# Kernel optimization log

Hardware: AMD Instinct MI355X
Metric: run time of the kernel (lower is better)

## Reference

```python
import jax, jax.numpy as jnp
import numpy as np

NUM_LAYER = 5
EMB = 256
N = 100000
E = 300000
SELF_LOOP_BOND = 4
BN_EPS = 1e-5


def setup_inputs() -> dict:
    key = jax.random.key(0)
    ks = jax.random.split(key, 16)
    f = lambda k, shape: jax.random.normal(k, shape, jnp.float32) * 0.02
    return {
        "x_atom": jax.random.randint(ks[0], (N,), 0, 120),
        "x_chir": jax.random.randint(ks[1], (N,), 0, 3),
        "edge_index": jax.random.randint(ks[2], (2, E), 0, N),
        "edge_bond": jax.random.randint(ks[3], (E,), 0, 4),
        "edge_dir": jax.random.randint(ks[4], (E,), 0, 3),
        "atom_emb": f(ks[5], (120, EMB)),
        "chir_emb": f(ks[6], (3, EMB)),
        "bond_embs": f(ks[7], (NUM_LAYER, 6, EMB)),
        "dir_embs": f(ks[8], (NUM_LAYER, 3, EMB)),
        "W1s": f(ks[9], (NUM_LAYER, 2 * EMB, EMB)),
        "b1s": f(ks[10], (NUM_LAYER, 2 * EMB)),
        "W2s": f(ks[11], (NUM_LAYER, EMB, 2 * EMB)),
        "b2s": f(ks[12], (NUM_LAYER, EMB)),
        "bn_w": jnp.ones((NUM_LAYER, EMB), jnp.float32),
        "bn_b": jnp.zeros((NUM_LAYER, EMB), jnp.float32),
    }


def reference(x_atom, x_chir, edge_index, edge_bond, edge_dir,
              atom_emb, chir_emb, bond_embs, dir_embs,
              W1s, b1s, W2s, b2s, bn_w, bn_b):
    n = x_atom.shape[0]
    src, dst = edge_index[0], edge_index[1]
    # add self loops (edge_attr = [4, 0] for each node)
    loop = jnp.arange(n)
    src_full = jnp.concatenate([src, loop])          # [E+N]
    dst_full = jnp.concatenate([dst, loop])          # [E+N]
    bond_full = jnp.concatenate([edge_bond, jnp.full((n,), SELF_LOOP_BOND, edge_bond.dtype)])
    dir_full = jnp.concatenate([edge_dir, jnp.zeros((n,), edge_dir.dtype)])

    # initial node features: atom + chirality embeddings
    h = atom_emb[x_atom] + chir_emb[x_chir]          # [N, EMB]

    for l in range(NUM_LAYER):
        # per-layer edge embeddings (bond type + bond direction)
        e_emb = bond_embs[l][bond_full] + dir_embs[l][dir_full]   # [E+N, EMB]
        # message = x_j + edge_attr; aggregate = scatter-add to dst
        msg = h[src_full] + e_emb                                  # gather
        agg = jax.ops.segment_sum(msg, dst_full, num_segments=n)  # scatter-add
        # update MLP: Linear(EMB->2EMB) -> ReLU -> Linear(2EMB->EMB)
        hmid = jax.nn.relu(agg @ W1s[l].T + b1s[l])                # [N, 2EMB]
        h2 = hmid @ W2s[l].T + b2s[l]                              # [N, EMB]
        # batch norm (training mode: batch statistics, biased variance)
        mean = h2.mean(axis=0)
        var = h2.var(axis=0)
        h2 = (h2 - mean) * jax.lax.rsqrt(var + BN_EPS) * bn_w[l] + bn_b[l]
        # relu on all but last layer; dropout with p=0 is identity
        if l < NUM_LAYER - 1:
            h2 = jax.nn.relu(h2)
        h = h2
    # JK == 'last'
    return h
```

## Files before the change

kernel.cpp:

```cpp
#include <hip/hip_runtime.h>

#define EMB 256
#define NLAYER 5
#define CHUNK 1024

typedef unsigned int u32;
typedef unsigned short u16;

typedef __bf16 bf16x8 __attribute__((ext_vector_type(8)));
typedef float f32x4 __attribute__((ext_vector_type(4)));

__device__ __forceinline__ float bf2f(u16 u) {
    union { u32 i; float f; } x; x.i = ((u32)u) << 16; return x.f;
}
__device__ __forceinline__ u16 f2bf(float f) {
    union { float f; u32 i; } x; x.f = f;
    u32 r = x.i + 0x7FFFu + ((x.i >> 16) & 1u);
    return (u16)(r >> 16);
}
__device__ __forceinline__ u32 cvt_pk_bf16(float lo, float hi) {
    u32 r;
    asm("v_cvt_pk_bf16_f32 %0, %1, %2" : "=v"(r) : "v"(lo), "v"(hi));
    return r;
}
__device__ __forceinline__ void unpack4(uint2 p, float* o) {
    union { u32 i; float f; } a, b, c, d;
    a.i = p.x << 16; b.i = p.x & 0xFFFF0000u;
    c.i = p.y << 16; d.i = p.y & 0xFFFF0000u;
    o[0] = a.f; o[1] = b.f; o[2] = c.f; o[3] = d.f;
}

#define GLOAD(dst, ptr) asm volatile("global_load_dwordx4 %0, %1, off" : "=&v"(dst) : "v"(ptr))
#define VMWAIT(n) asm volatile("s_waitcnt vmcnt(" #n ")" ::: "memory")

__global__ void k_detect(const u32* __restrict__ bnw_raw, int* __restrict__ flag) {
    if (threadIdx.x == 0 && blockIdx.x == 0)
        *flag = (bnw_raw[0] == 0x3F803F80u) ? 1 : 0;
}

struct Cvt { const void* s; u16* d; int n; };
struct CvtTab { Cvt t[10]; };

__global__ void k_convert(CvtTab tab, const int* __restrict__ flag, int maxn) {
    int f = *flag;
    int stride = gridDim.x * blockDim.x;
    for (int i = blockIdx.x * blockDim.x + threadIdx.x; i < maxn; i += stride) {
        for (int j = 0; j < 10; j++) {
            if (i < tab.t[j].n) {
                u16 v;
                if (f) v = ((const u16*)tab.t[j].s)[i];
                else   v = f2bf(((const float*)tab.t[j].s)[i]);
                tab.t[j].d[i] = v;
            }
        }
    }
}

__global__ void k_zero(u32* p, int n) {
    int i = blockIdx.x * blockDim.x + threadIdx.x;
    if (i < n) p[i] = 0u;
}

__global__ void k_hist(const int* __restrict__ eidx, const int* __restrict__ ebond,
                       const int* __restrict__ edir,
                       u32* __restrict__ cnt, u32* __restrict__ cntb, u32* __restrict__ cntd, int E) {
    int e = blockIdx.x * blockDim.x + threadIdx.x;
    if (e >= E) return;
    int dst = eidx[E + e];
    atomicAdd(&cnt[dst], 1u);
    atomicAdd(&cntb[dst * 4 + ebond[e]], 1u);
    atomicAdd(&cntd[dst * 3 + edir[e]], 1u);
}

__global__ void k_chunksum(const u32* __restrict__ cnt, u32* __restrict__ partial, int N) {
    int b = blockIdx.x, t = threadIdx.x;
    int base = b * CHUNK + t * 4;
    u32 s = 0;
    for (int i = 0; i < 4; i++) { int idx = base + i; if (idx < N) s += cnt[idx]; }
    __shared__ u32 red[256];
    red[t] = s; __syncthreads();
    for (int o = 128; o > 0; o >>= 1) { if (t < o) red[t] += red[t + o]; __syncthreads(); }
    if (t == 0) partial[b] = red[0];
}

__global__ void k_scanpartial(u32* partial, u32* indptr, int nch, int N) {
    if (threadIdx.x == 0 && blockIdx.x == 0) {
        u32 run = 0;
        for (int i = 0; i < nch; i++) { u32 x = partial[i]; partial[i] = run; run += x; }
        indptr[N] = run;
    }
}

__global__ void k_chunkscan(const u32* __restrict__ cnt, const u32* __restrict__ partial,
                            u32* __restrict__ indptr, u32* __restrict__ fillp, int N) {
    int b = blockIdx.x, t = threadIdx.x;
    int base = b * CHUNK + t * 4;
    u32 c[4]; u32 tsum = 0;
    for (int i = 0; i < 4; i++) { int idx = base + i; c[i] = (idx < N) ? cnt[idx] : 0u; tsum += c[i]; }
    __shared__ u32 sc[256];
    sc[t] = tsum; __syncthreads();
    for (int o = 1; o < 256; o <<= 1) {
        u32 x = (t >= o) ? sc[t - o] : 0u;
        __syncthreads();
        sc[t] += x;
        __syncthreads();
    }
    u32 run = partial[b] + sc[t] - tsum;
    for (int i = 0; i < 4; i++) {
        int idx = base + i;
        if (idx < N) { indptr[idx] = run; fillp[idx] = run; }
        run += c[i];
    }
}

__global__ void k_fill(const int* __restrict__ eidx, u32* __restrict__ fillp,
                       u32* __restrict__ srcs, int E) {
    int e = blockIdx.x * blockDim.x + threadIdx.x;
    if (e >= E) return;
    int dst = eidx[E + e];
    u32 pos = atomicAdd(&fillp[dst], 1u);
    srcs[pos] = (u32)eidx[e];
}

__global__ void k_h0(const int* __restrict__ xa, const int* __restrict__ xc,
                     const u16* __restrict__ aemb, const u16* __restrict__ cemb,
                     u16* __restrict__ H, int N) {
    int wave = threadIdx.x >> 6, lane = threadIdx.x & 63;
    int v = blockIdx.x * 4 + wave;
    if (v >= N) return;
    int a = xa[v], c = xc[v];
    int c4 = lane * 4;
    uint2 pa = *(const uint2*)(aemb + (size_t)a * EMB + c4);
    uint2 pc = *(const uint2*)(cemb + (size_t)c * EMB + c4);
    float fa[4], fc[4];
    unpack4(pa, fa); unpack4(pc, fc);
    ushort4 ov;
    ov.x = f2bf(fa[0] + fc[0]); ov.y = f2bf(fa[1] + fc[1]);
    ov.z = f2bf(fa[2] + fc[2]); ov.w = f2bf(fa[3] + fc[3]);
    *(ushort4*)(H + (size_t)v * EMB + c4) = ov;
}

#define KP 264
#define HSS 272

#define ACCROW(P)                                                     \
    {                                                                 \
        float f_[4]; unpack4(P, f_);                                  \
        _Pragma("unroll") for (int k_ = 0; k_ < 4; k_++) {            \
            float y_ = f_[k_] * sc[k_] + sh[k_];                      \
            if (relu) y_ = fmaxf(y_, 0.f);                            \
            acc[k_] += y_;                                            \
        }                                                             \
    }

#define G1STEP(BUF)                                                                              \
    {                                                                                            \
        _Pragma("unroll") for (int j = 0; j < 4; j++)                                            \
            _Pragma("unroll") for (int i = 0; i < 4; i++)                                        \
                acc1[i][j] = __builtin_amdgcn_mfma_f32_16x16x32_bf16(BUF[j], af[i], acc1[i][j], 0, 0, 0); \
        if (s + 3 < 8) {                                                                         \
            _Pragma("unroll") for (int j = 0; j < 4; j++)                                        \
                GLOAD(BUF[j], wp[j] + (s + 3) * 32);                                             \
        }                                                                                        \
    }

#define G2STEP(BUF)                                                                              \
    {                                                                                            \
        _Pragma("unroll") for (int i = 0; i < 4; i++)                                            \
            _Pragma("unroll") for (int j = 0; j < 4; j++)                                        \
                acc2[i][j] = __builtin_amdgcn_mfma_f32_16x16x32_bf16(hf[i], BUF[j], acc2[i][j], 0, 0, 0); \
        if (s + 3 < 8) {                                                                         \
            _Pragma("unroll") for (int j = 0; j < 4; j++)                                        \
                GLOAD(BUF[j], vp[j] + (s + 3) * 32);                                             \
        }                                                                                        \
    }

__global__ __launch_bounds__(256, 2) void k_fused(
    const u16* __restrict__ H, const u32* __restrict__ indptr, const u32* __restrict__ srcs,
    const u32* __restrict__ cntb, const u32* __restrict__ cntd,
    const u16* __restrict__ bemb, const u16* __restrict__ demb,
    const float* __restrict__ Sp, const u16* __restrict__ bnw, const u16* __restrict__ bnb,
    float invN, int relu,
    const u16* __restrict__ W1, const u16* __restrict__ b1,
    const u16* __restrict__ W2, const u16* __restrict__ b2,
    u16* __restrict__ C, float* __restrict__ S, int M) {
    __shared__ __align__(16) u16 As[64 * KP];
    __shared__ __align__(16) u16 Hs[64 * HSS];
    int m0 = blockIdx.x * 64;
    int t = threadIdx.x;
    int wave = t >> 6, lane = t & 63;
    int lr = lane & 15, quad = lane >> 4;
    int wq = wave * 64;
    int c4 = lane * 4;

    float sc[4] = {1.f, 1.f, 1.f, 1.f}, sh[4] = {0.f, 0.f, 0.f, 0.f};
    if (Sp) {
        float4 s0 = *(const float4*)(Sp + c4);
        float4 s1 = *(const float4*)(Sp + 256 + c4);
        ushort4 w4 = *(const ushort4*)(bnw + c4);
        ushort4 b4 = *(const ushort4*)(bnb + c4);
        float sv[4] = {s0.x, s0.y, s0.z, s0.w};
        float qv[4] = {s1.x, s1.y, s1.z, s1.w};
        u16 wv[4] = {w4.x, w4.y, w4.z, w4.w};
        u16 bv[4] = {b4.x, b4.y, b4.z, b4.w};
        #pragma unroll
        for (int k = 0; k < 4; k++) {
            float mean = sv[k] * invN;
            float var = fmaxf(qv[k] * invN - mean * mean, 0.f);
            float inv = rsqrtf(var + 1e-5f);
            sc[k] = bf2f(wv[k]) * inv;
            sh[k] = bf2f(bv[k]) - mean * sc[k];
        }
    }
    float eb[8][4];
    #pragma unroll
    for (int b = 0; b < 5; b++) { uint2 p = *(const uint2*)(bemb + b * EMB + c4); unpack4(p, eb[b]); }
    #pragma unroll
    for (int d = 0; d < 3; d++) { uint2 p = *(const uint2*)(demb + d * EMB + c4); unpack4(p, eb[5 + d]); }

    u32 nextbeg = 0;
    {
        int v0 = m0 + wave * 16;
        if (v0 < M) nextbeg = indptr[v0];
    }
    #pragma unroll 1
    for (int nn = 0; nn < 16; nn++) {
        int r = wave * 16 + nn;
        int v = m0 + r;
        float acc[4] = {0.f, 0.f, 0.f, 0.f};
        if (v < M) {
            u32 beg = nextbeg;
            u32 end = indptr[v + 1];
            nextbeg = end;
            uint2 pself = *(const uint2*)(H + (size_t)v * EMB + c4);
            float cb0 = (float)cntb[v * 4 + 0], cb1 = (float)cntb[v * 4 + 1];
            float cb2 = (float)cntb[v * 4 + 2], cb3 = (float)cntb[v * 4 + 3];
            float cd0 = (float)cntd[v * 3 + 0] + 1.f;
            float cd1 = (float)cntd[v * 3 + 1], cd2 = (float)cntd[v * 3 + 2];
            u32 e = beg;
            while (e < end) {
                u32 rem = end - e;
                u32 o1 = rem > 1 ? 1u : 0u, o2 = rem > 2 ? 2u : 0u, o3 = rem > 3 ? 3u : 0u;
                u32 i0 = srcs[e], i1 = srcs[e + o1], i2 = srcs[e + o2], i3 = srcs[e + o3];
                uint2 p0 = *(const uint2*)(H + (size_t)i0 * EMB + c4);
                uint2 p1 = *(const uint2*)(H + (size_t)i1 * EMB + c4);
                uint2 p2 = *(const uint2*)(H + (size_t)i2 * EMB + c4);
                uint2 p3 = *(const uint2*)(H + (size_t)i3 * EMB + c4);
                ACCROW(p0);
                if (rem > 1) ACCROW(p1);
                if (rem > 2) ACCROW(p2);
                if (rem > 3) ACCROW(p3);
                e += (rem < 4u) ? rem : 4u;
            }
            ACCROW(pself);
            #pragma unroll
            for (int k = 0; k < 4; k++)
                acc[k] += cb0 * eb[0][k] + cb1 * eb[1][k] + cb2 * eb[2][k] + cb3 * eb[3][k] + eb[4][k]
                        + cd0 * eb[5][k] + cd1 * eb[6][k] + cd2 * eb[7][k];
        }
        uint2 ov;
        ov.x = cvt_pk_bf16(acc[0], acc[1]);
        ov.y = cvt_pk_bf16(acc[2], acc[3]);
        *(uint2*)(As + r * KP + c4) = ov;
    }

    f32x4 acc2[4][4];
    #pragma unroll
    for (int i = 0; i < 4; i++)
        #pragma unroll
        for (int j = 0; j < 4; j++)
            acc2[i][j] = (f32x4){0.f, 0.f, 0.f, 0.f};

    __syncthreads();

    #pragma unroll
    for (int nh = 0; nh < 2; nh++) {
        f32x4 acc1[4][4];
        #pragma unroll
        for (int i = 0; i < 4; i++)
            #pragma unroll
            for (int j = 0; j < 4; j++)
                acc1[i][j] = (f32x4){0.f, 0.f, 0.f, 0.f};
        const u16* W1h = W1 + (size_t)(nh * 256) * 256;
        const u16* wp[4];
        #pragma unroll
        for (int j = 0; j < 4; j++)
            wp[j] = W1h + (size_t)(wq + j * 16 + lr) * 256 + quad * 8;

        bf16x8 wbA[4], wbB[4], wbC[4];
        #pragma unroll
        for (int j = 0; j < 4; j++) GLOAD(wbA[j], wp[j] + 0);
        #pragma unroll
        for (int j = 0; j < 4; j++) GLOAD(wbB[j], wp[j] + 32);
        #pragma unroll
        for (int j = 0; j < 4; j++) GLOAD(wbC[j], wp[j] + 64);

        #pragma unroll
        for (int s = 0; s < 8; s++) {
            bf16x8 af[4];
            #pragma unroll
            for (int i = 0; i < 4; i++)
                af[i] = *(const bf16x8*)(As + (i * 16 + lr) * KP + s * 32 + quad * 8);
            if (s < 6) { VMWAIT(8); } else if (s == 6) { VMWAIT(4); } else { VMWAIT(0); }
            __builtin_amdgcn_sched_barrier(0);
            if (s % 3 == 0)      G1STEP(wbA)
            else if (s % 3 == 1) G1STEP(wbB)
            else                 G1STEP(wbC)
        }
        __syncthreads();
        #pragma unroll
        for (int j = 0; j < 4; j++) {
            int wl = wq + j * 16 + quad * 4;
            ushort4 bq = *(const ushort4*)(b1 + nh * 256 + wl);
            float bv0 = bf2f(bq.x), bv1 = bf2f(bq.y), bv2 = bf2f(bq.z), bv3 = bf2f(bq.w);
            #pragma unroll
            for (int i = 0; i < 4; i++) {
                float v0 = fmaxf(acc1[i][j][0] + bv0, 0.f);
                float v1 = fmaxf(acc1[i][j][1] + bv1, 0.f);
                float v2 = fmaxf(acc1[i][j][2] + bv2, 0.f);
                float v3 = fmaxf(acc1[i][j][3] + bv3, 0.f);
                uint2 ov;
                ov.x = cvt_pk_bf16(v0, v1);
                ov.y = cvt_pk_bf16(v2, v3);
                *(uint2*)(Hs + (i * 16 + lr) * HSS + wl) = ov;
            }
        }
        __syncthreads();
        const u16* W2h = W2 + nh * 256;
        const u16* vp[4];
        #pragma unroll
        for (int j = 0; j < 4; j++)
            vp[j] = W2h + (size_t)(wq + j * 16 + lr) * 512 + quad * 8;

        bf16x8 vbA[4], vbB[4], vbC[4];
        #pragma unroll
        for (int j = 0; j < 4; j++) GLOAD(vbA[j], vp[j] + 0);
        #pragma unroll
        for (int j = 0; j < 4; j++) GLOAD(vbB[j], vp[j] + 32);
        #pragma unroll
        for (int j = 0; j < 4; j++) GLOAD(vbC[j], vp[j] + 64);

        #pragma unroll
        for (int s = 0; s < 8; s++) {
            bf16x8 hf[4];
            #pragma unroll
            for (int i = 0; i < 4; i++)
                hf[i] = *(const bf16x8*)(Hs + (i * 16 + lr) * HSS + s * 32 + quad * 8);
            if (s < 6) { VMWAIT(8); } else if (s == 6) { VMWAIT(4); } else { VMWAIT(0); }
            __builtin_amdgcn_sched_barrier(0);
            if (s % 3 == 0)      G2STEP(vbA)
            else if (s % 3 == 1) G2STEP(vbB)
            else                 G2STEP(vbC)
        }
    }

    #pragma unroll
    for (int j = 0; j < 4; j++) {
        int gn = wq + j * 16 + lr;
        float bv = bf2f(b2[gn]);
        float s = 0.f, q = 0.f;
        #pragma unroll
        for (int i = 0; i < 4; i++) {
            int mbase = m0 + i * 16 + quad * 4;
            #pragma unroll
            for (int r = 0; r < 4; r++) {
                int gm = mbase + r;
                if (gm < M) {
                    float v = acc2[i][j][r] + bv;
                    C[(size_t)gm * 256 + gn] = f2bf(v);
                    s += v; q += v * v;
                }
            }
        }
        s += __shfl_xor(s, 16, 64); s += __shfl_xor(s, 32, 64);
        q += __shfl_xor(q, 16, 64); q += __shfl_xor(q, 32, 64);
        if (quad == 0) {
            atomicAdd(&S[gn], s);
            atomicAdd(&S[256 + gn], q);
        }
    }
}

__global__ void k_out(const u16* __restrict__ H2, const float* __restrict__ Sp,
                      const u16* __restrict__ bnw, const u16* __restrict__ bnb, float invN,
                      void* __restrict__ out, const int* __restrict__ flag, int N) {
    int wave = threadIdx.x >> 6, lane = threadIdx.x & 63;
    int v = blockIdx.x * 4 + wave;
    if (v >= N) return;
    int c4 = lane * 4;
    float4 s0 = *(const float4*)(Sp + c4);
    float4 s1 = *(const float4*)(Sp + 256 + c4);
    ushort4 w4 = *(const ushort4*)(bnw + c4);
    ushort4 b4 = *(const ushort4*)(bnb + c4);
    float sv[4] = {s0.x, s0.y, s0.z, s0.w};
    float qv[4] = {s1.x, s1.y, s1.z, s1.w};
    u16 wv[4] = {w4.x, w4.y, w4.z, w4.w};
    u16 bv[4] = {b4.x, b4.y, b4.z, b4.w};
    float sc[4], sh[4];
    #pragma unroll
    for (int k = 0; k < 4; k++) {
        float mean = sv[k] * invN;
        float var = fmaxf(qv[k] * invN - mean * mean, 0.f);
        float inv = rsqrtf(var + 1e-5f);
        sc[k] = bf2f(wv[k]) * inv;
        sh[k] = bf2f(bv[k]) - mean * sc[k];
    }
    uint2 p = *(const uint2*)(H2 + (size_t)v * EMB + c4);
    float f[4]; unpack4(p, f);
    float o0 = f[0] * sc[0] + sh[0];
    float o1 = f[1] * sc[1] + sh[1];
    float o2 = f[2] * sc[2] + sh[2];
    float o3 = f[3] * sc[3] + sh[3];
    if (*flag) {
        ushort4 ov;
        ov.x = f2bf(o0); ov.y = f2bf(o1); ov.z = f2bf(o2); ov.w = f2bf(o3);
        *(ushort4*)((u16*)out + (size_t)v * EMB + c4) = ov;
    } else {
        float4 ov = make_float4(o0, o1, o2, o3);
        *(float4*)((float*)out + (size_t)v * EMB + c4) = ov;
    }
}

extern "C" void kernel_launch(void* const* d_in, const int* in_sizes, int n_in,
                              void* d_out, int out_size, void* d_ws, size_t ws_size,
                              hipStream_t stream) {
    const int* x_atom = (const int*)d_in[0];
    const int* x_chir = (const int*)d_in[1];
    const int* eidx   = (const int*)d_in[2];
    const int* ebond  = (const int*)d_in[3];
    const int* edir   = (const int*)d_in[4];

    const int N = in_sizes[0];
    const int E = in_sizes[3];

    char* p = (char*)d_ws;
    size_t off = 0;
    auto alloc = [&](size_t bytes) -> void* {
        void* r = p + off;
        off += bytes;
        off = (off + 255) & ~(size_t)255;
        return r;
    };
    u16* X   = (u16*)alloc((size_t)N * EMB * 2);
    u16* Y   = (u16*)alloc((size_t)N * EMB * 2);
    u32* cz  = (u32*)alloc(((size_t)8 * N + NLAYER * 512) * 4);
    u32* cnt  = cz;
    u32* cntb = cz + N;
    u32* cntd = cz + 5 * (size_t)N;
    float* stats5 = (float*)(cz + 8 * (size_t)N);
    u32* indptr = (u32*)alloc((size_t)(N + 1) * 4);
    u32* fillp  = (u32*)alloc((size_t)N * 4);
    u32* srcs   = (u32*)alloc((size_t)E * 4);
    u32* partial = (u32*)alloc(256 * 4);
    int* flag    = (int*)alloc(256);

    int csz[10] = {120 * EMB, 3 * EMB, NLAYER * 6 * EMB, NLAYER * 3 * EMB,
                   NLAYER * 512 * EMB, NLAYER * 512, NLAYER * EMB * 512, NLAYER * EMB,
                   NLAYER * EMB, NLAYER * EMB};
    u16* cbuf[10];
    for (int j = 0; j < 10; j++) cbuf[j] = (u16*)alloc((size_t)csz[j] * 2);
    u16* atom_emb  = cbuf[0];
    u16* chir_emb  = cbuf[1];
    u16* bond_embs = cbuf[2];
    u16* dir_embs  = cbuf[3];
    u16* W1s = cbuf[4];
    u16* b1s = cbuf[5];
    u16* W2s = cbuf[6];
    u16* b2s = cbuf[7];
    u16* bnw = cbuf[8];
    u16* bnb = cbuf[9];

    const int nodeBlocks = (N + 3) / 4;
    const int nch = (N + CHUNK - 1) / CHUNK;

    k_detect<<<1, 64, 0, stream>>>((const u32*)d_in[13], flag);
    {
        CvtTab tab;
        int maxn = 0;
        for (int j = 0; j < 10; j++) {
            tab.t[j].s = d_in[5 + j];
            tab.t[j].d = cbuf[j];
            tab.t[j].n = csz[j];
            if (csz[j] > maxn) maxn = csz[j];
        }
        k_convert<<<(maxn + 255) / 256, 256, 0, stream>>>(tab, flag, maxn);
    }

    {
        int z = 8 * N + NLAYER * 512;
        k_zero<<<(z + 255) / 256, 256, 0, stream>>>(cz, z);
    }
    k_hist<<<(E + 255) / 256, 256, 0, stream>>>(eidx, ebond, edir, cnt, cntb, cntd, E);
    k_chunksum<<<nch, 256, 0, stream>>>(cnt, partial, N);
    k_scanpartial<<<1, 64, 0, stream>>>(partial, indptr, nch, N);
    k_chunkscan<<<nch, 256, 0, stream>>>(cnt, partial, indptr, fillp, N);
    k_fill<<<(E + 255) / 256, 256, 0, stream>>>(eidx, fillp, srcs, E);

    k_h0<<<nodeBlocks, 256, 0, stream>>>(x_atom, x_chir, atom_emb, chir_emb, X, N);

    u16* H = X;
    u16* O = Y;
    const int mT64 = (N + 63) / 64;
    const float invN = 1.0f / (float)N;
    for (int l = 0; l < NLAYER; l++) {
        const u16* bemb = bond_embs + (size_t)l * 6 * EMB;
        const u16* demb = dir_embs + (size_t)l * 3 * EMB;
        const u16* W1 = W1s + (size_t)l * 512 * EMB;
        const u16* B1 = b1s + (size_t)l * 512;
        const u16* W2 = W2s + (size_t)l * EMB * 512;
        const u16* B2 = b2s + (size_t)l * EMB;
        float* stats = stats5 + (size_t)l * 512;
        const float* Sprev = (l == 0) ? nullptr : stats5 + (size_t)(l - 1) * 512;
        const u16* bw = bnw + (size_t)(l ? l - 1 : 0) * EMB;
        const u16* bb = bnb + (size_t)(l ? l - 1 : 0) * EMB;

        k_fused<<<mT64, 256, 0, stream>>>(H, indptr, srcs, cntb, cntd, bemb, demb,
                                          Sprev, bw, bb, invN, (l == 0) ? 0 : 1,
                                          W1, B1, W2, B2, O, stats, N);
        u16* tmp = H; H = O; O = tmp;
    }

    k_out<<<nodeBlocks, 256, 0, stream>>>(H, stats5 + (size_t)4 * 512,
                                          bnw + (size_t)4 * EMB, bnb + (size_t)4 * EMB, invN,
                                          d_out, flag, N);
}
```

Before: 1.400 ms.

## Split neighbor aggregation into separate kernel and double-buffer MFMA fragment loads

Moves the gather/segment-sum, previous-layer BN and ReLU, and edge-embedding accumulation out of the MFMA-heavy fused MLP kernel into a standalone high-occupancy k_scatter kernel with one node per wave. The aggregated bf16 rows are written to global memory, then staged into LDS by the MLP kernel, which writes its output in place. The aim is to stop latency-bound irregular gathers running at the low occupancy the MLP kernel's LDS and register budget allows. It also prefetches the next A/H fragments from LDS with even/odd double-buffering and raises wave priority around MFMA bursts. The cost is an extra global round-trip of the aggregated activations and one more launch per layer.

Measured after the change: 1.198 ms. -14.5%, faster.

```diff
diff --git a/kernel.cpp b/kernel.cpp
--- a/kernel.cpp
+++ b/kernel.cpp
@@ -140,9 +140,6 @@
     *(ushort4*)(H + (size_t)v * EMB + c4) = ov;
 }
 
-#define KP 264
-#define HSS 272
-
 #define ACCROW(P)                                                     \
     {                                                                 \
         float f_[4]; unpack4(P, f_);                                  \
@@ -153,46 +150,23 @@
         }                                                             \
     }
 
-#define G1STEP(BUF)                                                                              \
-    {                                                                                            \
-        _Pragma("unroll") for (int j = 0; j < 4; j++)                                            \
-            _Pragma("unroll") for (int i = 0; i < 4; i++)                                        \
-                acc1[i][j] = __builtin_amdgcn_mfma_f32_16x16x32_bf16(BUF[j], af[i], acc1[i][j], 0, 0, 0); \
-        if (s + 3 < 8) {                                                                         \
-            _Pragma("unroll") for (int j = 0; j < 4; j++)                                        \
-                GLOAD(BUF[j], wp[j] + (s + 3) * 32);                                             \
-        }                                                                                        \
-    }
-
-#define G2STEP(BUF)                                                                              \
-    {                                                                                            \
-        _Pragma("unroll") for (int i = 0; i < 4; i++)                                            \
-            _Pragma("unroll") for (int j = 0; j < 4; j++)                                        \
-                acc2[i][j] = __builtin_amdgcn_mfma_f32_16x16x32_bf16(hf[i], BUF[j], acc2[i][j], 0, 0, 0); \
-        if (s + 3 < 8) {                                                                         \
-            _Pragma("unroll") for (int j = 0; j < 4; j++)                                        \
-                GLOAD(BUF[j], vp[j] + (s + 3) * 32);                                             \
-        }                                                                                        \
-    }
-
-__global__ __launch_bounds__(256, 2) void k_fused(
-    const u16* __restrict__ H, const u32* __restrict__ indptr, const u32* __restrict__ srcs,
-    const u32* __restrict__ cntb, const u32* __restrict__ cntd,
-    const u16* __restrict__ bemb, const u16* __restrict__ demb,
-    const float* __restrict__ Sp, const u16* __restrict__ bnw, const u16* __restrict__ bnb,
-    float invN, int relu,
-    const u16* __restrict__ W1, const u16* __restrict__ b1,
-    const u16* __restrict__ W2, const u16* __restrict__ b2,
-    u16* __restrict__ C, float* __restrict__ S, int M) {
-    __shared__ __align__(16) u16 As[64 * KP];
-    __shared__ __align__(16) u16 Hs[64 * HSS];
-    int m0 = blockIdx.x * 64;
-    int t = threadIdx.x;
-    int wave = t >> 6, lane = t & 63;
-    int lr = lane & 15, quad = lane >> 4;
-    int wq = wave * 64;
+__global__ void k_scatter(const u16* __restrict__ H, const u32* __restrict__ indptr,
+                          const u32* __restrict__ srcs,
+                          const u32* __restrict__ cntb, const u32* __restrict__ cntd,
+                          const u16* __restrict__ bemb, const u16* __restrict__ demb,
+                          const float* __restrict__ Sp, const u16* __restrict__ bnw,
+                          const u16* __restrict__ bnb, float invN, int relu,
+                          u16* __restrict__ AGG, int N) {
+    int wave = threadIdx.x >> 6, lane = threadIdx.x & 63;
+    int v = blockIdx.x * 4 + wave;
+    if (v >= N) return;
     int c4 = lane * 4;
-
+    u32 beg = indptr[v], end = indptr[v + 1];
+    uint2 pself = *(const uint2*)(H + (size_t)v * EMB + c4);
+    float cb0 = (float)cntb[v * 4 + 0], cb1 = (float)cntb[v * 4 + 1];
+    float cb2 = (float)cntb[v * 4 + 2], cb3 = (float)cntb[v * 4 + 3];
+    float cd0 = (float)cntd[v * 3 + 0] + 1.f;
+    float cd1 = (float)cntd[v * 3 + 1], cd2 = (float)cntd[v * 3 + 2];
     float sc[4] = {1.f, 1.f, 1.f, 1.f}, sh[4] = {0.f, 0.f, 0.f, 0.f};
     if (Sp) {
         float4 s0 = *(const float4*)(Sp + c4);
@@ -218,50 +192,79 @@
     #pragma unroll
     for (int d = 0; d < 3; d++) { uint2 p = *(const uint2*)(demb + d * EMB + c4); unpack4(p, eb[5 + d]); }
 
-    u32 nextbeg = 0;
-    {
-        int v0 = m0 + wave * 16;
-        if (v0 < M) nextbeg = indptr[v0];
-    }
-    #pragma unroll 1
-    for (int nn = 0; nn < 16; nn++) {
-        int r = wave * 16 + nn;
-        int v = m0 + r;
-        float acc[4] = {0.f, 0.f, 0.f, 0.f};
-        if (v < M) {
-            u32 beg = nextbeg;
-            u32 end = indptr[v + 1];
-            nextbeg = end;
-            uint2 pself = *(const uint2*)(H + (size_t)v * EMB + c4);
-            float cb0 = (float)cntb[v * 4 + 0], cb1 = (float)cntb[v * 4 + 1];
-            float cb2 = (float)cntb[v * 4 + 2], cb3 = (float)cntb[v * 4 + 3];
-            float cd0 = (float)cntd[v * 3 + 0] + 1.f;
-            float cd1 = (float)cntd[v * 3 + 1], cd2 = (float)cntd[v * 3 + 2];
-            u32 e = beg;
-            while (e < end) {
-                u32 rem = end - e;
-                u32 o1 = rem > 1 ? 1u : 0u, o2 = rem > 2 ? 2u : 0u, o3 = rem > 3 ? 3u : 0u;
-                u32 i0 = srcs[e], i1 = srcs[e + o1], i2 = srcs[e + o2], i3 = srcs[e + o3];
-                uint2 p0 = *(const uint2*)(H + (size_t)i0 * EMB + c4);
-                uint2 p1 = *(const uint2*)(H + (size_t)i1 * EMB + c4);
-                uint2 p2 = *(const uint2*)(H + (size_t)i2 * EMB + c4);
-                uint2 p3 = *(const uint2*)(H + (size_t)i3 * EMB + c4);
-                ACCROW(p0);
-                if (rem > 1) ACCROW(p1);
-                if (rem > 2) ACCROW(p2);
-                if (rem > 3) ACCROW(p3);
-                e += (rem < 4u) ? rem : 4u;
-            }
-            ACCROW(pself);
-            #pragma unroll
-            for (int k = 0; k < 4; k++)
-                acc[k] += cb0 * eb[0][k] + cb1 * eb[1][k] + cb2 * eb[2][k] + cb3 * eb[3][k] + eb[4][k]
-                        + cd0 * eb[5][k] + cd1 * eb[6][k] + cd2 * eb[7][k];
-        }
-        uint2 ov;
-        ov.x = cvt_pk_bf16(acc[0], acc[1]);
-        ov.y = cvt_pk_bf16(acc[2], acc[3]);
-        *(uint2*)(As + r * KP + c4) = ov;
+    float acc[4] = {0.f, 0.f, 0.f, 0.f};
+    u32 e = beg;
+    while (e < end) {
+        u32 rem = end - e;
+        u32 o1 = rem > 1 ? 1u : 0u, o2 = rem > 2 ? 2u : 0u, o3 = rem > 3 ? 3u : 0u;
+        u32 i0 = srcs[e], i1 = srcs[e + o1], i2 = srcs[e + o2], i3 = srcs[e + o3];
+        uint2 p0 = *(const uint2*)(H + (size_t)i0 * EMB + c4);
+        uint2 p1 = *(const uint2*)(H + (size_t)i1 * EMB + c4);
+        uint2 p2 = *(const uint2*)(H + (size_t)i2 * EMB + c4);
+        uint2 p3 = *(const uint2*)(H + (size_t)i3 * EMB + c4);
+        ACCROW(p0);
+        if (rem > 1) ACCROW(p1);
+        if (rem > 2) ACCROW(p2);
+        if (rem > 3) ACCROW(p3);
+        e += (rem < 4u) ? rem : 4u;
+    }
+    ACCROW(pself);
+    #pragma unroll
+    for (int k = 0; k < 4; k++)
+        acc[k] += cb0 * eb[0][k] + cb1 * eb[1][k] + cb2 * eb[2][k] + cb3 * eb[3][k] + eb[4][k]
+                + cd0 * eb[5][k] + cd1 * eb[6][k] + cd2 * eb[7][k];
+    uint2 ov;
+    ov.x = cvt_pk_bf16(acc[0], acc[1]);
+    ov.y = cvt_pk_bf16(acc[2], acc[3]);
+    *(uint2*)(AGG + (size_t)v * EMB + c4) = ov;
+}
+
+#define KP 264
+#define HSS 272
+
+#define G1STEP(BUF, AF)                                                                          \
+    {                                                                                            \
+        __builtin_amdgcn_s_setprio(1);                                                           \
+        _Pragma("unroll") for (int j = 0; j < 4; j++)                                            \
+            _Pragma("unroll") for (int i = 0; i < 4; i++)                                        \
+                acc1[i][j] = __builtin_amdgcn_mfma_f32_16x16x32_bf16(BUF[j], AF[i], acc1[i][j], 0, 0, 0); \
+        __builtin_amdgcn_s_setprio(0);                                                           \
+        if (s + 3 < 8) {                                                                         \
+            _Pragma("unroll") for (int j = 0; j < 4; j++)                                        \
+                GLOAD(BUF[j], wp[j] + (s + 3) * 32);                                             \
+        }                                                                                        \
+    }
+
+#define G2STEP(BUF, HF)                                                                          \
+    {                                                                                            \
+        __builtin_amdgcn_s_setprio(1);                                                           \
+        _Pragma("unroll") for (int i = 0; i < 4; i++)                                            \
+            _Pragma("unroll") for (int j = 0; j < 4; j++)                                        \
+                acc2[i][j] = __builtin_amdgcn_mfma_f32_16x16x32_bf16(HF[i], BUF[j], acc2[i][j], 0, 0, 0); \
+        __builtin_amdgcn_s_setprio(0);                                                           \
+        if (s + 3 < 8) {                                                                         \
+            _Pragma("unroll") for (int j = 0; j < 4; j++)                                        \
+                GLOAD(BUF[j], vp[j] + (s + 3) * 32);                                             \
+        }                                                                                        \
+    }
+
+__global__ __launch_bounds__(256, 2) void k_fused(
+    const u16* __restrict__ A, const u16* __restrict__ W1, const u16* __restrict__ b1,
+    const u16* __restrict__ W2, const u16* __restrict__ b2,
+    u16* __restrict__ C, float* __restrict__ S, int M) {
+    __shared__ __align__(16) u16 As[64 * KP];
+    __shared__ __align__(16) u16 Hs[64 * HSS];
+    int m0 = blockIdx.x * 64;
+    int t = threadIdx.x;
+    int wave = t >> 6, lane = t & 63;
+    int lr = lane & 15, quad = lane >> 4;
+    int wq = wave * 64;
+
+    for (int it = 0; it < 8; it++) {
+        int ci = t + it * 256;
+        int r = ci >> 5, kc = (ci & 31) * 8;
+        int gr = m0 + r; if (gr > M - 1) gr = M - 1;
+        *(uint4*)(As + r * KP + kc) = *(const uint4*)(A + (size_t)gr * 256 + kc);
     }
 
     f32x4 acc2[4][4];
@@ -295,17 +298,35 @@
         #pragma unroll
         for (int j = 0; j < 4; j++) GLOAD(wbC[j], wp[j] + 64);
 
+        bf16x8 afE[4], afO[4];
+        #pragma unroll
+        for (int i = 0; i < 4; i++)
+            afE[i] = *(const bf16x8*)(As + (i * 16 + lr) * KP + quad * 8);
+
         #pragma unroll
         for (int s = 0; s < 8; s++) {
-            bf16x8 af[4];
-            #pragma unroll
-            for (int i = 0; i < 4; i++)
-                af[i] = *(const bf16x8*)(As + (i * 16 + lr) * KP + s * 32 + quad * 8);
+            if (s < 7) {
+                if ((s & 1) == 0) {
+                    #pragma unroll
+                    for (int i = 0; i < 4; i++)
+                        afO[i] = *(const bf16x8*)(As + (i * 16 + lr) * KP + (s + 1) * 32 + quad * 8);
+                } else {
+                    #pragma unroll
+                    for (int i = 0; i < 4; i++)
+                        afE[i] = *(const bf16x8*)(As + (i * 16 + lr) * KP + (s + 1) * 32 + quad * 8);
+                }
+            }
             if (s < 6) { VMWAIT(8); } else if (s == 6) { VMWAIT(4); } else { VMWAIT(0); }
             __builtin_amdgcn_sched_barrier(0);
-            if (s % 3 == 0)      G1STEP(wbA)
-            else if (s % 3 == 1) G1STEP(wbB)
-            else                 G1STEP(wbC)
+            if ((s & 1) == 0) {
+                if (s % 3 == 0)      G1STEP(wbA, afE)
+                else if (s % 3 == 1) G1STEP(wbB, afE)
+                else                 G1STEP(wbC, afE)
+            } else {
+                if (s % 3 == 0)      G1STEP(wbA, afO)
+                else if (s % 3 == 1) G1STEP(wbB, afO)
+                else                 G1STEP(wbC, afO)
+            }
         }
         __syncthreads();
         #pragma unroll
@@ -340,17 +361,35 @@
         #pragma unroll
         for (int j = 0; j < 4; j++) GLOAD(vbC[j], vp[j] + 64);
 
+        bf16x8 hfE[4], hfO[4];
+        #pragma unroll
+        for (int i = 0; i < 4; i++)
+            hfE[i] = *(const bf16x8*)(Hs + (i * 16 + lr) * HSS + quad * 8);
+
         #pragma unroll
         for (int s = 0; s < 8; s++) {
-            bf16x8 hf[4];
-            #pragma unroll
-            for (int i = 0; i < 4; i++)
-                hf[i] = *(const bf16x8*)(Hs + (i * 16 + lr) * HSS + s * 32 + quad * 8);
+            if (s < 7) {
+                if ((s & 1) == 0) {
+                    #pragma unroll
+                    for (int i = 0; i < 4; i++)
+                        hfO[i] = *(const bf16x8*)(Hs + (i * 16 + lr) * HSS + (s + 1) * 32 + quad * 8);
+                } else {
+                    #pragma unroll
+                    for (int i = 0; i < 4; i++)
+                        hfE[i] = *(const bf16x8*)(Hs + (i * 16 + lr) * HSS + (s + 1) * 32 + quad * 8);
+                }
+            }
             if (s < 6) { VMWAIT(8); } else if (s == 6) { VMWAIT(4); } else { VMWAIT(0); }
             __builtin_amdgcn_sched_barrier(0);
-            if (s % 3 == 0)      G2STEP(vbA)
-            else if (s % 3 == 1) G2STEP(vbB)
-            else                 G2STEP(vbC)
+            if ((s & 1) == 0) {
+                if (s % 3 == 0)      G2STEP(vbA, hfE)
+                else if (s % 3 == 1) G2STEP(vbB, hfE)
+                else                 G2STEP(vbC, hfE)
+            } else {
+                if (s % 3 == 0)      G2STEP(vbA, hfO)
+                else if (s % 3 == 1) G2STEP(vbB, hfO)
+                else                 G2STEP(vbC, hfO)
+            }
         }
     }
 
@@ -499,7 +538,7 @@
     k_h0<<<nodeBlocks, 256, 0, stream>>>(x_atom, x_chir, atom_emb, chir_emb, X, N);
 
     u16* H = X;
-    u16* O = Y;
+    u16* A = Y;
     const int mT64 = (N + 63) / 64;
     const float invN = 1.0f / (float)N;
     for (int l = 0; l < NLAYER; l++) {
@@ -514,10 +553,11 @@
         const u16* bw = bnw + (size_t)(l ? l - 1 : 0) * EMB;
         const u16* bb = bnb + (size_t)(l ? l - 1 : 0) * EMB;
 
-        k_fused<<<mT64, 256, 0, stream>>>(H, indptr, srcs, cntb, cntd, bemb, demb,
-                                          Sprev, bw, bb, invN, (l == 0) ? 0 : 1,
-                                          W1, B1, W2, B2, O, stats, N);
-        u16* tmp = H; H = O; O = tmp;
+        k_scatter<<<nodeBlocks, 256, 0, stream>>>(H, indptr, srcs, cntb, cntd, bemb, demb,
+                                                  Sprev, bw, bb, invN, (l == 0) ? 0 : 1,
+                                                  A, N);
+        k_fused<<<mT64, 256, 0, stream>>>(A, W1, B1, W2, B2, A, stats, N);
+        u16* tmp = H; H = A; A = tmp;
     }
 
     k_out<<<nodeBlocks, 256, 0, stream>>>(H, stats5 + (size_t)4 * 512,
```
